# Optimization experiments

Measured on AMD Instinct MI355X. Metric: run time of the kernel, lower is better.

The kernel has to match this reference:

```python
import jax, jax.numpy as jnp
import numpy as np

N = 256
NH = 256  # GRU hidden units
K = 2     # local Hilbert space dim (hardcoded in module)


def gru_step(x, h, Wk, Wr, b):
    # TF keras GRU, reset_after=True, gate order (z, r, h)
    gx = x @ Wk + b[0]          # [B, 3*NH]
    gh = h @ Wr + b[1]          # [B, 3*NH]
    xz, xr, xh = jnp.split(gx, 3, axis=-1)
    hz, hr, hn = jnp.split(gh, 3, axis=-1)
    z = jax.nn.sigmoid(xz + hz)
    r = jax.nn.sigmoid(xr + hr)
    hh = jnp.tanh(xh + r * hn)
    return z * h + (1.0 - z) * hh


def setup_inputs() -> dict:
    key = jax.random.key(0)
    k1, k2, k3 = jax.random.split(key, 3)
    return {
        "gru_kernel": jax.random.normal(k1, (K, 3 * NH), jnp.float32) * 0.05,
        "gru_rec_kernel": jax.random.normal(k2, (NH, 3 * NH), jnp.float32) * 0.05,
        "gru_bias": jnp.zeros((2, 3 * NH), jnp.float32),
        "dense_kernel": jax.random.normal(k3, (NH, K), jnp.float32) * 0.05,
        "dense_bias": jnp.zeros((K,), jnp.float32),
        "nsamples": 2048,
    }


def reference(gru_kernel, gru_rec_kernel, gru_bias, dense_kernel, dense_bias, nsamples):
    keys = jax.random.split(jax.random.key(42), N)
    x0 = jnp.zeros((nsamples, K), jnp.float32)      # 0 * one_hot(0) == zeros
    h0 = jnp.zeros((nsamples, NH), jnp.float32)
    logP0 = jnp.zeros((nsamples,), jnp.float32)

    def step(carry, key):
        x, h, logP = carry
        h = gru_step(x, h, gru_kernel, gru_rec_kernel, gru_bias)
        probs = jax.nn.softmax(h @ dense_kernel + dense_bias, axis=-1)  # [B, K]
        log_probs = jnp.log(1e-10 + probs)
        s = jax.random.categorical(key, log_probs, axis=-1)             # [B]
        onehot = jax.nn.one_hot(s, K, dtype=jnp.float32)
        logP = logP + jnp.sum(log_probs * onehot, axis=1)
        return (onehot, h, logP), s

    (_, _, logP), samples = jax.lax.scan(step, (x0, h0, logP0), keys)
    samples = samples.T.astype(jnp.int32)  # [nsamples, N]
    return samples, logP
```

## Files before the change

### kernel.cpp

```cpp
#include <hip/hip_runtime.h>
#include <stdint.h>

#define NSTEPS 256
#define NHID   256
#define NG     768
#define BPB    8
#define TPB    768
#define NSAMP  2048

__device__ __forceinline__ uint32_t rotl32(uint32_t v, int r){ return (v<<r)|(v>>(32-r)); }

__device__ __forceinline__ void tf2x32(uint32_t k0, uint32_t k1,
                                       uint32_t x0, uint32_t x1,
                                       uint32_t& o0, uint32_t& o1){
  const uint32_t ks2 = k0 ^ k1 ^ 0x1BD11BDAu;
  x0 += k0; x1 += k1;
#define TF_R(r) { x0 += x1; x1 = rotl32(x1,(r)); x1 ^= x0; }
  TF_R(13) TF_R(15) TF_R(26) TF_R(6)
  x0 += k1;  x1 += ks2 + 1u;
  TF_R(17) TF_R(29) TF_R(16) TF_R(24)
  x0 += ks2; x1 += k0 + 2u;
  TF_R(13) TF_R(15) TF_R(26) TF_R(6)
  x0 += k0;  x1 += k1 + 3u;
  TF_R(17) TF_R(29) TF_R(16) TF_R(24)
  x0 += k1;  x1 += ks2 + 4u;
  TF_R(13) TF_R(15) TF_R(26) TF_R(6)
  x0 += ks2; x1 += k0 + 5u;
#undef TF_R
  o0 = x0; o1 = x1;
}

__device__ __forceinline__ float tanh_xla(float x){
  float xc = fminf(fmaxf(x, -9.0f), 9.0f);
  float x2 = xc*xc;
  float p = -2.76076847742355e-16f;
  p = fmaf(p, x2, 2.00018790482477e-13f);
  p = fmaf(p, x2, -8.60467152213735e-11f);
  p = fmaf(p, x2, 5.12229709037114e-08f);
  p = fmaf(p, x2, 1.48572235717979e-05f);
  p = fmaf(p, x2, 6.37261928875436e-04f);
  p = fmaf(p, x2, 4.89352455891786e-03f);
  p = p * xc;
  float q = 1.19825839466702e-06f;
  q = fmaf(q, x2, 1.18534705686654e-04f);
  q = fmaf(q, x2, 2.26843463243900e-03f);
  q = fmaf(q, x2, 4.89352518554385e-03f);
  float r = p / q;
  return (fabsf(x) < 0.0004f) ? x : r;
}

__device__ __forceinline__ float sigmoid_ref(float x){
  return fmaf(0.5f, tanh_xla(0.5f*x), 0.5f);
}

__global__ __launch_bounds__(TPB, 3) void rnn_sampler(
    const float* __restrict__ Wk,
    const float* __restrict__ Wr,
    const float* __restrict__ Bias,
    const float* __restrict__ Dk,
    const float* __restrict__ Db,
    float* __restrict__ out)
{
  __shared__ float    h_lds[BPB][NHID];
  __shared__ float    part[2][BPB][NG];
  __shared__ uint32_t key0[NSTEPS];
  __shared__ uint32_t key1[NSTEPS];
  __shared__ int      xsel[BPB];
  __shared__ float    logP[BPB];

  const int tid  = threadIdx.x;
  const int b    = blockIdx.x;
  const int ks   = tid / 192;
  const int cq   = tid % 192;
  const int wid  = tid >> 6;
  const int lane = tid & 63;

  if (tid < NSTEPS) {
    uint32_t o0, o1;
    tf2x32(0u, 42u, 0u, (uint32_t)tid, o0, o1);
    key0[tid] = o0; key1[tid] = o1;
  }
  for (int i = tid; i < BPB*NHID; i += TPB) (&h_lds[0][0])[i] = 0.0f;
  if (tid < BPB) { xsel[tid] = 0; logP[tid] = 0.0f; }
  __syncthreads();

  const int k0 = ks * 64;
  const float* wp = Wr + (size_t)k0 * NG + 4*cq;
  float4 acc[BPB];

  for (int t = 0; t <= NSTEPS; ++t) {
    if (t > 0 && wid < BPB) {
      const int tc = t - 1;
      const int s  = wid;
      float4 h4 = *(const float4*)&h_lds[s][lane * 4];
      const float4* dk4 = (const float4*)(Dk + lane * 8);
      float4 d0 = dk4[0], d1 = dk4[1];
      float a0 = h4.x*d0.x + h4.y*d0.z + h4.z*d1.x + h4.w*d1.z;
      float a1 = h4.x*d0.y + h4.y*d0.w + h4.z*d1.y + h4.w*d1.w;
#pragma unroll
      for (int off = 32; off > 0; off >>= 1) {
        a0 += __shfl_down(a0, off);
        a1 += __shfl_down(a1, off);
      }
      if (lane == 0) {
        float l0 = a0 + Db[0], l1 = a1 + Db[1];
        float m  = fmaxf(l0, l1);
        float e0 = expf(l0 - m), e1 = expf(l1 - m);
        float sum = e0 + e1;
        float p0 = e0 / sum, p1 = e1 / sum;
        float lp0 = logf(1e-10f + p0), lp1 = logf(1e-10f + p1);

        const int i = b * BPB + s;
        const uint32_t kA = key0[tc], kB = key1[tc];
        uint32_t o0, o1;
        tf2x32(kA, kB, 0u, (uint32_t)(2*i),     o0, o1);
        uint32_t bits0 = o0 ^ o1;
        tf2x32(kA, kB, 0u, (uint32_t)(2*i + 1), o0, o1);
        uint32_t bits1 = o0 ^ o1;

        const float TINY = 1.17549435e-38f;
        float u0 = __uint_as_float((bits0 >> 9) | 0x3f800000u) - 1.0f;
        float u1 = __uint_as_float((bits1 >> 9) | 0x3f800000u) - 1.0f;
        u0 = fmaxf(TINY, u0 * (1.0f - TINY) + TINY);
        u1 = fmaxf(TINY, u1 * (1.0f - TINY) + TINY);
        float g0 = -logf(-logf(u0));
        float g1 = -logf(-logf(u1));

        float v0 = g0 + lp0, v1 = g1 + lp1;
        int st = (v1 > v0) ? 1 : 0;
        logP[s] += st ? lp1 : lp0;
        xsel[s] = 1 + st;
        out[(size_t)i * NSTEPS + tc] = (float)st;
      }
    }
    if (t == NSTEPS) break;

#pragma unroll
    for (int s = 0; s < BPB; ++s) acc[s] = make_float4(0.f, 0.f, 0.f, 0.f);

#pragma unroll 2
    for (int kk = 0; kk < 64; kk += 4) {
      const float* rp = wp + (size_t)kk * NG;
      float4 w0 = *(const float4*)(rp);
      float4 w1 = *(const float4*)(rp + NG);
      float4 w2 = *(const float4*)(rp + 2*NG);
      float4 w3 = *(const float4*)(rp + 3*NG);
#pragma unroll
      for (int s = 0; s < BPB; ++s) {
        float4 h4 = *(const float4*)&h_lds[s][k0 + kk];
        acc[s].x = fmaf(h4.x, w0.x, acc[s].x);
        acc[s].y = fmaf(h4.x, w0.y, acc[s].y);
        acc[s].z = fmaf(h4.x, w0.z, acc[s].z);
        acc[s].w = fmaf(h4.x, w0.w, acc[s].w);
        acc[s].x = fmaf(h4.y, w1.x, acc[s].x);
        acc[s].y = fmaf(h4.y, w1.y, acc[s].y);
        acc[s].z = fmaf(h4.y, w1.z, acc[s].z);
        acc[s].w = fmaf(h4.y, w1.w, acc[s].w);
        acc[s].x = fmaf(h4.z, w2.x, acc[s].x);
        acc[s].y = fmaf(h4.z, w2.y, acc[s].y);
        acc[s].z = fmaf(h4.z, w2.z, acc[s].z);
        acc[s].w = fmaf(h4.z, w2.w, acc[s].w);
        acc[s].x = fmaf(h4.w, w3.x, acc[s].x);
        acc[s].y = fmaf(h4.w, w3.y, acc[s].y);
        acc[s].z = fmaf(h4.w, w3.z, acc[s].z);
        acc[s].w = fmaf(h4.w, w3.w, acc[s].w);
      }
    }
    if (ks >= 2) {
#pragma unroll
      for (int s = 0; s < BPB; ++s)
        *(float4*)&part[ks-2][s][4*cq] = acc[s];
    }
    __syncthreads();
    if (ks < 2) {
#pragma unroll
      for (int s = 0; s < BPB; ++s) {
        float4 p = *(const float4*)&part[ks][s][4*cq];
        p.x += acc[s].x; p.y += acc[s].y; p.z += acc[s].z; p.w += acc[s].w;
        *(float4*)&part[ks][s][4*cq] = p;
      }
    }
    __syncthreads();

    for (int item = tid; item < NSAMP; item += TPB) {
      int s = item >> 8, n = item & 255;
      float ghz = (part[0][s][n]     + part[1][s][n])     + Bias[NG + n];
      float ghr = (part[0][s][n+256] + part[1][s][n+256]) + Bias[NG + n + 256];
      float ghn = (part[0][s][n+512] + part[1][s][n+512]) + Bias[NG + n + 512];
      int xs = xsel[s];
      float gxz, gxr, gxh;
      if (xs == 0) {
        gxz = Bias[n]; gxr = Bias[n+256]; gxh = Bias[n+512];
      } else {
        const float* wkrow = Wk + (size_t)(xs - 1) * NG;
        gxz = wkrow[n]     + Bias[n];
        gxr = wkrow[n+256] + Bias[n+256];
        gxh = wkrow[n+512] + Bias[n+512];
      }
      float z  = sigmoid_ref(gxz + ghz);
      float r  = sigmoid_ref(gxr + ghr);
      float hh = tanh_xla(gxh + r * ghn);
      float ho = h_lds[s][n];
      h_lds[s][n] = z * ho + (1.0f - z) * hh;
    }
    __syncthreads();
  }

  __syncthreads();

  if (tid < BPB) {
    const int i = b * BPB + tid;
    out[(size_t)NSAMP * NSTEPS + i] = logP[tid];
  }
}

extern "C" void kernel_launch(void* const* d_in, const int* in_sizes, int n_in,
                              void* d_out, int out_size, void* d_ws, size_t ws_size,
                              hipStream_t stream) {
  const float* Wk = (const float*)d_in[0];
  const float* Wr = (const float*)d_in[1];
  const float* B  = (const float*)d_in[2];
  const float* Dk = (const float*)d_in[3];
  const float* Db = (const float*)d_in[4];
  float* out = (float*)d_out;
  rnn_sampler<<<dim3(NSAMP / BPB), dim3(TPB), 0, stream>>>(Wk, Wr, B, Dk, Db, out);
}
```

Before: 3.393 ms.

## Use four partial buffers, software-pipeline weight loads, stage constants in LDS

All four K-slices now write their partial sums to separate LDS buffers. This removes the read-add-write pass and one barrier per step, and the elementwise stage sums all four partials. The recurrent matvec loop is manually double-buffered so that the next group's weight and h loads are issued before the current group's FMAs. Wk, bias, dense kernel and dense bias are cached in LDS. The two Threefry/Gumbel draws per sample now run in parallel on two lanes instead of serially on one. The cost is much more LDS (partial buffers double) and more registers for the double-buffered operands, which can reduce occupancy.

```diff
diff --git a/kernel.cpp b/kernel.cpp
--- a/kernel.cpp
+++ b/kernel.cpp
@@ -53,6 +53,17 @@
   return fmaf(0.5f, tanh_xla(0.5f*x), 0.5f);
 }
 
+__device__ __forceinline__ void gfma(float4 h, float4 w0, float4 w1, float4 w2, float4 w3, float4& a){
+  a.x = fmaf(h.x, w0.x, a.x); a.y = fmaf(h.x, w0.y, a.y);
+  a.z = fmaf(h.x, w0.z, a.z); a.w = fmaf(h.x, w0.w, a.w);
+  a.x = fmaf(h.y, w1.x, a.x); a.y = fmaf(h.y, w1.y, a.y);
+  a.z = fmaf(h.y, w1.z, a.z); a.w = fmaf(h.y, w1.w, a.w);
+  a.x = fmaf(h.z, w2.x, a.x); a.y = fmaf(h.z, w2.y, a.y);
+  a.z = fmaf(h.z, w2.z, a.z); a.w = fmaf(h.z, w2.w, a.w);
+  a.x = fmaf(h.w, w3.x, a.x); a.y = fmaf(h.w, w3.y, a.y);
+  a.z = fmaf(h.w, w3.z, a.z); a.w = fmaf(h.w, w3.w, a.w);
+}
+
 __global__ __launch_bounds__(TPB, 3) void rnn_sampler(
     const float* __restrict__ Wk,
     const float* __restrict__ Wr,
@@ -62,11 +73,15 @@
     float* __restrict__ out)
 {
   __shared__ float    h_lds[BPB][NHID];
-  __shared__ float    part[2][BPB][NG];
+  __shared__ float    part[4][BPB][NG];
   __shared__ uint32_t key0[NSTEPS];
   __shared__ uint32_t key1[NSTEPS];
+  __shared__ float    wk_lds[2*NG];
+  __shared__ float    bias_lds[2*NG];
+  __shared__ float    dk_lds[NHID*2];
+  __shared__ float    db_lds[2];
   __shared__ int      xsel[BPB];
-  __shared__ float    logP[BPB];
+  __shared__ float    logPs[BPB];
 
   const int tid  = threadIdx.x;
   const int b    = blockIdx.x;
@@ -81,7 +96,10 @@
     key0[tid] = o0; key1[tid] = o1;
   }
   for (int i = tid; i < BPB*NHID; i += TPB) (&h_lds[0][0])[i] = 0.0f;
-  if (tid < BPB) { xsel[tid] = 0; logP[tid] = 0.0f; }
+  for (int i = tid; i < 2*NG; i += TPB) { wk_lds[i] = Wk[i]; bias_lds[i] = Bias[i]; }
+  for (int i = tid; i < NHID*2; i += TPB) dk_lds[i] = Dk[i];
+  if (tid < 2) db_lds[tid] = Db[tid];
+  if (tid < BPB) { xsel[tid] = 0; logPs[tid] = 0.0f; }
   __syncthreads();
 
   const int k0 = ks * 64;
@@ -93,8 +111,8 @@
       const int tc = t - 1;
       const int s  = wid;
       float4 h4 = *(const float4*)&h_lds[s][lane * 4];
-      const float4* dk4 = (const float4*)(Dk + lane * 8);
-      float4 d0 = dk4[0], d1 = dk4[1];
+      float4 d0 = *(const float4*)&dk_lds[lane * 8];
+      float4 d1 = *(const float4*)&dk_lds[lane * 8 + 4];
       float a0 = h4.x*d0.x + h4.y*d0.z + h4.z*d1.x + h4.w*d1.z;
       float a1 = h4.x*d0.y + h4.y*d0.w + h4.z*d1.y + h4.w*d1.w;
 #pragma unroll
@@ -102,34 +120,30 @@
         a0 += __shfl_down(a0, off);
         a1 += __shfl_down(a1, off);
       }
+      float gv = 0.0f;
+      if (lane < 2) {
+        const int i = b * BPB + s;
+        uint32_t o0, o1;
+        tf2x32(key0[tc], key1[tc], 0u, (uint32_t)(2*i + lane), o0, o1);
+        uint32_t bits = o0 ^ o1;
+        const float TINY = 1.17549435e-38f;
+        float u = __uint_as_float((bits >> 9) | 0x3f800000u) - 1.0f;
+        u = fmaxf(TINY, u * (1.0f - TINY) + TINY);
+        gv = -logf(-logf(u));
+      }
+      float g1 = __shfl(gv, 1);
       if (lane == 0) {
-        float l0 = a0 + Db[0], l1 = a1 + Db[1];
+        float l0 = a0 + db_lds[0], l1 = a1 + db_lds[1];
         float m  = fmaxf(l0, l1);
         float e0 = expf(l0 - m), e1 = expf(l1 - m);
         float sum = e0 + e1;
         float p0 = e0 / sum, p1 = e1 / sum;
         float lp0 = logf(1e-10f + p0), lp1 = logf(1e-10f + p1);
-
+        float v0 = gv + lp0, v1 = g1 + lp1;
+        int st = (v1 > v0) ? 1 : 0;
+        logPs[s] += st ? lp1 : lp0;
+        xsel[s] = 1 + st;
         const int i = b * BPB + s;
-        const uint32_t kA = key0[tc], kB = key1[tc];
-        uint32_t o0, o1;
-        tf2x32(kA, kB, 0u, (uint32_t)(2*i),     o0, o1);
-        uint32_t bits0 = o0 ^ o1;
-        tf2x32(kA, kB, 0u, (uint32_t)(2*i + 1), o0, o1);
-        uint32_t bits1 = o0 ^ o1;
-
-        const float TINY = 1.17549435e-38f;
-        float u0 = __uint_as_float((bits0 >> 9) | 0x3f800000u) - 1.0f;
-        float u1 = __uint_as_float((bits1 >> 9) | 0x3f800000u) - 1.0f;
-        u0 = fmaxf(TINY, u0 * (1.0f - TINY) + TINY);
-        u1 = fmaxf(TINY, u1 * (1.0f - TINY) + TINY);
-        float g0 = -logf(-logf(u0));
-        float g1 = -logf(-logf(u1));
-
-        float v0 = g0 + lp0, v1 = g1 + lp1;
-        int st = (v1 > v0) ? 1 : 0;
-        logP[s] += st ? lp1 : lp0;
-        xsel[s] = 1 + st;
         out[(size_t)i * NSTEPS + tc] = (float)st;
       }
     }
@@ -138,64 +152,72 @@
 #pragma unroll
     for (int s = 0; s < BPB; ++s) acc[s] = make_float4(0.f, 0.f, 0.f, 0.f);
 
-#pragma unroll 2
-    for (int kk = 0; kk < 64; kk += 4) {
-      const float* rp = wp + (size_t)kk * NG;
-      float4 w0 = *(const float4*)(rp);
-      float4 w1 = *(const float4*)(rp + NG);
-      float4 w2 = *(const float4*)(rp + 2*NG);
-      float4 w3 = *(const float4*)(rp + 3*NG);
-#pragma unroll
-      for (int s = 0; s < BPB; ++s) {
-        float4 h4 = *(const float4*)&h_lds[s][k0 + kk];
-        acc[s].x = fmaf(h4.x, w0.x, acc[s].x);
-        acc[s].y = fmaf(h4.x, w0.y, acc[s].y);
-        acc[s].z = fmaf(h4.x, w0.z, acc[s].z);
-        acc[s].w = fmaf(h4.x, w0.w, acc[s].w);
-        acc[s].x = fmaf(h4.y, w1.x, acc[s].x);
-        acc[s].y = fmaf(h4.y, w1.y, acc[s].y);
-        acc[s].z = fmaf(h4.y, w1.z, acc[s].z);
-        acc[s].w = fmaf(h4.y, w1.w, acc[s].w);
-        acc[s].x = fmaf(h4.z, w2.x, acc[s].x);
-        acc[s].y = fmaf(h4.z, w2.y, acc[s].y);
-        acc[s].z = fmaf(h4.z, w2.z, acc[s].z);
-        acc[s].w = fmaf(h4.z, w2.w, acc[s].w);
-        acc[s].x = fmaf(h4.w, w3.x, acc[s].x);
-        acc[s].y = fmaf(h4.w, w3.y, acc[s].y);
-        acc[s].z = fmaf(h4.w, w3.z, acc[s].z);
-        acc[s].w = fmaf(h4.w, w3.w, acc[s].w);
-      }
-    }
-    if (ks >= 2) {
-#pragma unroll
-      for (int s = 0; s < BPB; ++s)
-        *(float4*)&part[ks-2][s][4*cq] = acc[s];
-    }
+    float4 wA0, wA1, wA2, wA3, wB0, wB1, wB2, wB3;
+    float4 hA[BPB], hB[BPB];
+    {
+      const float* rp = wp;
+      wA0 = *(const float4*)(rp);
+      wA1 = *(const float4*)(rp + NG);
+      wA2 = *(const float4*)(rp + 2*NG);
+      wA3 = *(const float4*)(rp + 3*NG);
+    }
+#pragma unroll
+    for (int s = 0; s < BPB; ++s) hA[s] = *(const float4*)&h_lds[s][k0];
+
+    for (int g = 0; g < 16; g += 2) {
+      {
+        const float* rp = wp + (size_t)((g + 1) * 4) * NG;
+        wB0 = *(const float4*)(rp);
+        wB1 = *(const float4*)(rp + NG);
+        wB2 = *(const float4*)(rp + 2*NG);
+        wB3 = *(const float4*)(rp + 3*NG);
+      }
+#pragma unroll
+      for (int s = 0; s < BPB; ++s) hB[s] = *(const float4*)&h_lds[s][k0 + 4*(g+1)];
+#pragma unroll
+      for (int s = 0; s < BPB; ++s) gfma(hA[s], wA0, wA1, wA2, wA3, acc[s]);
+
+      const int g2 = (g + 2 < 16) ? (g + 2) : 0;
+      {
+        const float* rp = wp + (size_t)(g2 * 4) * NG;
+        wA0 = *(const float4*)(rp);
+        wA1 = *(const float4*)(rp + NG);
+        wA2 = *(const float4*)(rp + 2*NG);
+        wA3 = *(const float4*)(rp + 3*NG);
+      }
+#pragma unroll
+      for (int s = 0; s < BPB; ++s) hA[s] = *(const float4*)&h_lds[s][k0 + 4*g2];
+#pragma unroll
+      for (int s = 0; s < BPB; ++s) gfma(hB[s], wB0, wB1, wB2, wB3, acc[s]);
+    }
+
+#pragma unroll
+    for (int s = 0; s < BPB; ++s)
+      *(float4*)&part[ks][s][4*cq] = acc[s];
     __syncthreads();
-    if (ks < 2) {
-#pragma unroll
-      for (int s = 0; s < BPB; ++s) {
-        float4 p = *(const float4*)&part[ks][s][4*cq];
-        p.x += acc[s].x; p.y += acc[s].y; p.z += acc[s].z; p.w += acc[s].w;
-        *(float4*)&part[ks][s][4*cq] = p;
-      }
-    }
-    __syncthreads();
-
-    for (int item = tid; item < NSAMP; item += TPB) {
+
+#pragma unroll
+    for (int it = 0; it < 3; ++it) {
+      int item;
+      if (it == 0)      item = tid;
+      else if (it == 1) item = tid + TPB;
+      else {
+        if (tid < 256) break;
+        item = 1280 + tid;
+      }
       int s = item >> 8, n = item & 255;
-      float ghz = (part[0][s][n]     + part[1][s][n])     + Bias[NG + n];
-      float ghr = (part[0][s][n+256] + part[1][s][n+256]) + Bias[NG + n + 256];
-      float ghn = (part[0][s][n+512] + part[1][s][n+512]) + Bias[NG + n + 512];
+      float ghz = ((part[0][s][n]     + part[2][s][n])     + (part[1][s][n]     + part[3][s][n]))     + bias_lds[NG + n];
+      float ghr = ((part[0][s][n+256] + part[2][s][n+256]) + (part[1][s][n+256] + part[3][s][n+256])) + bias_lds[NG + n + 256];
+      float ghn = ((part[0][s][n+512] + part[2][s][n+512]) + (part[1][s][n+512] + part[3][s][n+512])) + bias_lds[NG + n + 512];
       int xs = xsel[s];
       float gxz, gxr, gxh;
       if (xs == 0) {
-        gxz = Bias[n]; gxr = Bias[n+256]; gxh = Bias[n+512];
+        gxz = bias_lds[n]; gxr = bias_lds[n+256]; gxh = bias_lds[n+512];
       } else {
-        const float* wkrow = Wk + (size_t)(xs - 1) * NG;
-        gxz = wkrow[n]     + Bias[n];
-        gxr = wkrow[n+256] + Bias[n+256];
-        gxh = wkrow[n+512] + Bias[n+512];
+        const float* wkrow = wk_lds + (xs - 1) * NG;
+        gxz = wkrow[n]     + bias_lds[n];
+        gxr = wkrow[n+256] + bias_lds[n+256];
+        gxh = wkrow[n+512] + bias_lds[n+512];
       }
       float z  = sigmoid_ref(gxz + ghz);
       float r  = sigmoid_ref(gxr + ghr);
@@ -210,7 +232,7 @@
 
   if (tid < BPB) {
     const int i = b * BPB + tid;
-    out[(size_t)NSAMP * NSTEPS + i] = logP[tid];
+    out[(size_t)NSAMP * NSTEPS + i] = logPs[tid];
   }
 }
 
```

After: 3.140 ms. 7.5% less time.
